# Performance work log

Measured on AMD Instinct MI355X. Metric: run time of the kernel, lower is better.

## Reference

```python
import jax, jax.numpy as jnp
import numpy as np

N_EMBD = 1024
N_HEAD = 16
B, T = 4, 2048

def setup_inputs() -> dict:
    key = jax.random.key(0)
    ks = jax.random.split(key, 5)
    C = N_EMBD
    s = 0.02
    return {
        "x": jax.random.normal(ks[0], (B, T, C), dtype=jnp.float32),
        "W_attn": jax.random.normal(ks[1], (C, 3 * C), dtype=jnp.float32) * s,
        "b_attn": jnp.zeros((3 * C,), dtype=jnp.float32),
        "W_proj": jax.random.normal(ks[2], (C, C), dtype=jnp.float32) * s,
        "b_proj": jnp.zeros((C,), dtype=jnp.float32),
    }

def reference(x, W_attn, b_attn, W_proj, b_proj):
    Bz, Tz, C = x.shape
    H = N_HEAD
    hd = C // H
    qkv = x @ W_attn + b_attn                      # [B,T,3C]
    q, k, v = jnp.split(qkv, 3, axis=-1)
    # [B,H,T,hd]
    q = q.reshape(Bz, Tz, H, hd).transpose(0, 2, 1, 3)
    k = k.reshape(Bz, Tz, H, hd).transpose(0, 2, 1, 3)
    v = v.reshape(Bz, Tz, H, hd).transpose(0, 2, 1, 3)
    att = jnp.einsum('bhqd,bhkd->bhqk', q, k) * (1.0 / np.sqrt(hd))
    causal = jnp.tril(jnp.ones((Tz, Tz), dtype=bool))
    att = jnp.where(causal, att, -jnp.inf)
    att = jax.nn.softmax(att, axis=-1)
    y = jnp.einsum('bhqk,bhkd->bhqd', att, v)      # [B,H,T,hd]
    y = y.transpose(0, 2, 1, 3).reshape(Bz, Tz, C)
    return y @ W_proj + b_proj
```

## Files before the change

### kernel.cpp

```cpp
#include <hip/hip_runtime.h>
#include <hip/hip_bf16.h>

#define NEMBD 1024
#define NHEAD 16
#define HD    64
#define BB    4
#define TT    2048
#define MM    (BB*TT)
#define NQKV  (3*NEMBD)

typedef unsigned short u16;
typedef __attribute__((ext_vector_type(8))) short short8;
typedef __attribute__((ext_vector_type(4))) float floatx4;

__device__ __forceinline__ u16 f2bf(float f) {
    __hip_bfloat16 h = __float2bfloat16(f);
    return *reinterpret_cast<u16*>(&h);
}

__device__ __forceinline__ unsigned pack_bf16(float a, float b) {
    __hip_bfloat162 h2 = __float22bfloat162_rn(float2{a, b});
    return *reinterpret_cast<unsigned*>(&h2);
}

__device__ __forceinline__ void gl_lds16(const u16* g, u16* l) {
    __builtin_amdgcn_global_load_lds(
        (const __attribute__((address_space(1))) unsigned int*)g,
        (__attribute__((address_space(3))) unsigned int*)l,
        16, 0, 0);
}

__global__ __launch_bounds__(256) void cast_f32_bf16(const float* __restrict__ in,
                                                     u16* __restrict__ out, int n) {
    int i = (blockIdx.x * 256 + threadIdx.x) * 4;
    if (i < n) {
        float4 v = *(const float4*)(in + i);
        uint2 o;
        o.x = pack_bf16(v.x, v.y);
        o.y = pack_bf16(v.z, v.w);
        *(uint2*)(out + i) = o;
    }
}

__global__ __launch_bounds__(256) void transpose_cast(const float* __restrict__ in,
                                                      u16* __restrict__ out, int K, int N) {
    __shared__ float tile[32][33];
    int n0 = blockIdx.x * 32, k0 = blockIdx.y * 32;
    int tx = threadIdx.x, ty = threadIdx.y;
    for (int i = 0; i < 4; i++)
        tile[ty + i * 8][tx] = in[(k0 + ty + i * 8) * N + n0 + tx];
    __syncthreads();
    for (int i = 0; i < 4; i++)
        out[(n0 + ty + i * 8) * K + k0 + tx] = f2bf(tile[tx][ty + i * 8]);
}

template <int EPI>
__global__ __launch_bounds__(256)
void gemm_bt(const u16* __restrict__ A, const u16* __restrict__ Bt,
             const float* __restrict__ bias, void* __restrict__ out0,
             u16* __restrict__ outK, u16* __restrict__ outV) {
    const int K = NEMBD;
    __shared__ u16 As[128 * 32];
    __shared__ u16 Bs[128 * 32];
    int tid = threadIdx.x;
    int lane = tid & 63, w = tid >> 6;
    int quad = lane >> 4, l16 = lane & 15;
    int wm = w >> 1, wn = w & 1;
    int bM = blockIdx.y * 128, bN = blockIdx.x * 128;

    floatx4 acc[4][4];
    for (int i = 0; i < 4; i++)
        for (int j = 0; j < 4; j++)
            acc[i][j] = (floatx4){0.f, 0.f, 0.f, 0.f};

    int srow = lane >> 2, scol = (lane & 3) * 8;
    const u16* Ag0 = A  + (size_t)(bM + w * 32 + srow) * K + scol;
    const u16* Ag1 = A  + (size_t)(bM + w * 32 + 16 + srow) * K + scol;
    const u16* Bg0 = Bt + (size_t)(bN + w * 32 + srow) * K + scol;
    const u16* Bg1 = Bt + (size_t)(bN + w * 32 + 16 + srow) * K + scol;
    u16* LA0 = &As[(w * 32) * 32];
    u16* LA1 = &As[(w * 32 + 16) * 32];
    u16* LB0 = &Bs[(w * 32) * 32];
    u16* LB1 = &Bs[(w * 32 + 16) * 32];

    for (int k0 = 0; k0 < K; k0 += 32) {
        gl_lds16(Ag0 + k0, LA0);
        gl_lds16(Ag1 + k0, LA1);
        gl_lds16(Bg0 + k0, LB0);
        gl_lds16(Bg1 + k0, LB1);
        __syncthreads();
        short8 af[4], bf[4];
        for (int i = 0; i < 4; i++)
            af[i] = *(const short8*)&As[(wm * 64 + i * 16 + l16) * 32 + quad * 8];
        for (int j = 0; j < 4; j++)
            bf[j] = *(const short8*)&Bs[(wn * 64 + j * 16 + l16) * 32 + quad * 8];
        for (int i = 0; i < 4; i++)
            for (int j = 0; j < 4; j++)
                acc[i][j] = __builtin_amdgcn_mfma_f32_16x16x32_bf16(af[i], bf[j], acc[i][j], 0, 0, 0);
        __syncthreads();
    }

    for (int i = 0; i < 4; i++) {
        int mbase = bM + wm * 64 + i * 16 + quad * 4;
        for (int j = 0; j < 4; j++) {
            int n = bN + wn * 64 + j * 16 + l16;
            float bv = bias[n];
            for (int r = 0; r < 4; r++) {
                float v = acc[i][j][r] + bv;
                int mg = mbase + r;
                if (EPI == 0) {
                    int which = n >> 10, c = n & 1023;
                    int h = c >> 6, d = c & 63;
                    int b = mg >> 11, t = mg & 2047;
                    u16* dst = (which == 0) ? (u16*)out0 : (which == 1 ? outK : outV);
                    dst[(((size_t)(b * NHEAD + h) * TT) + t) * HD + d] = f2bf(v);
                } else {
                    ((float*)out0)[(size_t)mg * NEMBD + n] = v;
                }
            }
        }
    }
}

__global__ __launch_bounds__(256)
void attn_kernel(const u16* __restrict__ Q, const u16* __restrict__ Kg,
                 const u16* __restrict__ V, u16* __restrict__ Y) {
    __shared__ u16 Ks[64][72];
    __shared__ u16 Vt[64][72];
    __shared__ u16 Ps[4][32][40];

    int tid = threadIdx.x;
    int lane = tid & 63, w = tid >> 6;
    int quad = lane >> 4, l16 = lane & 15;
    int bh = blockIdx.y;
    int ib = blockIdx.x;
    int qa0 = ib * 128;
    int qb0 = (15 - ib) * 128;
    const u16* Qb = Q  + (size_t)bh * TT * HD;
    const u16* Kb = Kg + (size_t)bh * TT * HD;
    const u16* Vb = V  + (size_t)bh * TT * HD;
    int wqa = qa0 + w * 32;
    int wqb = qb0 + w * 32;

    short8 qfa[2][2], qfb[2][2];
    for (int qt = 0; qt < 2; qt++)
        for (int kd = 0; kd < 2; kd++) {
            qfa[qt][kd] = *(const short8*)(Qb + (size_t)(wqa + qt * 16 + l16) * HD + kd * 32 + quad * 8);
            qfb[qt][kd] = *(const short8*)(Qb + (size_t)(wqb + qt * 16 + l16) * HD + kd * 32 + quad * 8);
        }

    floatx4 oa[4][2], ob[4][2];
    for (int dt = 0; dt < 4; dt++)
        for (int qt = 0; qt < 2; qt++) {
            oa[dt][qt] = (floatx4){0.f, 0.f, 0.f, 0.f};
            ob[dt][qt] = (floatx4){0.f, 0.f, 0.f, 0.f};
        }
    float la[2] = {0.f, 0.f};
    float lb[2] = {0.f, 0.f};

    const float C = 0.18033688f;

    int krow = tid >> 2, kcg = (tid & 3) * 16;
    int vkp = (tid & 31) * 2, vd0 = (tid >> 5) * 8;

    auto process = [&](int k0, int wq0, short8 (&qf)[2][2], floatx4 (&o)[4][2],
                       float (&l_s)[2]) {
        if (k0 >= wq0 + 32) return;
        short8 kf[4][2];
        for (int kt = 0; kt < 4; kt++)
            for (int kd = 0; kd < 2; kd++)
                kf[kt][kd] = *(const short8*)&Ks[kt * 16 + l16][kd * 32 + quad * 8];
        floatx4 s[2][4];
        for (int qt = 0; qt < 2; qt++)
            for (int kt = 0; kt < 4; kt++) {
                floatx4 a = (floatx4){0.f, 0.f, 0.f, 0.f};
                a = __builtin_amdgcn_mfma_f32_16x16x32_bf16(kf[kt][0], qf[qt][0], a, 0, 0, 0);
                a = __builtin_amdgcn_mfma_f32_16x16x32_bf16(kf[kt][1], qf[qt][1], a, 0, 0, 0);
                s[qt][kt] = a;
            }

        bool diag = (k0 + 64 > wq0);
        for (int qt = 0; qt < 2; qt++) {
            int qg = wq0 + qt * 16 + l16;
            if (diag) {
                for (int kt = 0; kt < 4; kt++)
                    for (int r = 0; r < 4; r++)
                        if (k0 + kt * 16 + quad * 4 + r > qg) s[qt][kt][r] = -INFINITY;
            }
            float rs = 0.f;
            for (int kt = 0; kt < 4; kt++)
                for (int r = 0; r < 4; r++) {
                    float p = exp2f(s[qt][kt][r] * C);
                    s[qt][kt][r] = p;
                    rs += p;
                }
            l_s[qt] += rs;
        }

        for (int c = 0; c < 2; c++) {
            for (int qt = 0; qt < 2; qt++)
                for (int ktl = 0; ktl < 2; ktl++) {
                    floatx4 p = s[qt][c * 2 + ktl];
                    *(unsigned*)&Ps[w][qt * 16 + l16][ktl * 16 + quad * 4]     = pack_bf16(p[0], p[1]);
                    *(unsigned*)&Ps[w][qt * 16 + l16][ktl * 16 + quad * 4 + 2] = pack_bf16(p[2], p[3]);
                }
            short8 pfrag[2];
            for (int qt = 0; qt < 2; qt++)
                pfrag[qt] = *(const short8*)&Ps[w][qt * 16 + l16][quad * 8];
            for (int dt = 0; dt < 4; dt++) {
                short8 vfrag = *(const short8*)&Vt[dt * 16 + l16][c * 32 + quad * 8];
                for (int qt = 0; qt < 2; qt++)
                    o[dt][qt] = __builtin_amdgcn_mfma_f32_16x16x32_bf16(vfrag, pfrag[qt], o[dt][qt], 0, 0, 0);
            }
        }
    };

    int kend = qb0 + 128;
    for (int k0 = 0; k0 < kend; k0 += 64) {
        *(uint4*)&Ks[krow][kcg]     = *(const uint4*)(Kb + (size_t)(k0 + krow) * HD + kcg);
        *(uint4*)&Ks[krow][kcg + 8] = *(const uint4*)(Kb + (size_t)(k0 + krow) * HD + kcg + 8);
        uint4 v0 = *(const uint4*)(Vb + (size_t)(k0 + vkp) * HD + vd0);
        uint4 v1 = *(const uint4*)(Vb + (size_t)(k0 + vkp + 1) * HD + vd0);
        const u16* e0 = (const u16*)&v0;
        const u16* e1 = (const u16*)&v1;
        for (int e = 0; e < 8; e++) {
            unsigned pk = (unsigned)e0[e] | ((unsigned)e1[e] << 16);
            *(unsigned*)&Vt[vd0 + e][vkp] = pk;
        }
        __syncthreads();

        if (k0 < qa0 + 128) process(k0, wqa, qfa, oa, la);
        process(k0, wqb, qfb, ob, lb);

        __syncthreads();
    }

    int b = bh >> 4, h = bh & 15;
    for (int half = 0; half < 2; half++) {
        floatx4 (&o)[4][2] = half ? ob : oa;
        float* l_s = half ? lb : la;
        int wq0 = half ? wqb : wqa;
        for (int qt = 0; qt < 2; qt++) {
            float lt = l_s[qt];
            lt += __shfl_xor(lt, 16, 64);
            lt += __shfl_xor(lt, 32, 64);
            float inv = 1.0f / lt;
            int qg = wq0 + qt * 16 + l16;
            size_t base = ((size_t)(b * TT + qg)) * NEMBD + h * HD;
            for (int dt = 0; dt < 4; dt++) {
                *(unsigned*)&Y[base + dt * 16 + quad * 4]     = pack_bf16(o[dt][qt][0] * inv, o[dt][qt][1] * inv);
                *(unsigned*)&Y[base + dt * 16 + quad * 4 + 2] = pack_bf16(o[dt][qt][2] * inv, o[dt][qt][3] * inv);
            }
        }
    }
}

extern "C" void kernel_launch(void* const* d_in, const int* in_sizes, int n_in,
                              void* d_out, int out_size, void* d_ws, size_t ws_size,
                              hipStream_t stream) {
    const float* x      = (const float*)d_in[0];
    const float* W_attn = (const float*)d_in[1];
    const float* b_attn = (const float*)d_in[2];
    const float* W_proj = (const float*)d_in[3];
    const float* b_proj = (const float*)d_in[4];
    float* out = (float*)d_out;

    char* ws = (char*)d_ws;
    u16* xb  = (u16*)(ws + 0);
    u16* wat = (u16*)(ws + 16777216);
    u16* wpt = (u16*)(ws + 23068672);
    u16* Qb  = (u16*)(ws + 25165824);
    u16* Kb  = (u16*)(ws + 41943040);
    u16* Vb  = (u16*)(ws + 58720256);

    cast_f32_bf16<<<(MM * NEMBD / 4 + 255) / 256, 256, 0, stream>>>(x, xb, MM * NEMBD);
    dim3 tb(32, 8);
    transpose_cast<<<dim3(NQKV / 32, NEMBD / 32), tb, 0, stream>>>(W_attn, wat, NEMBD, NQKV);
    transpose_cast<<<dim3(NEMBD / 32, NEMBD / 32), tb, 0, stream>>>(W_proj, wpt, NEMBD, NEMBD);

    gemm_bt<0><<<dim3(NQKV / 128, MM / 128), 256, 0, stream>>>(xb, wat, b_attn, (void*)Qb, Kb, Vb);
    attn_kernel<<<dim3(8, BB * NHEAD), 256, 0, stream>>>(Qb, Kb, Vb, xb);
    gemm_bt<1><<<dim3(NEMBD / 128, MM / 128), 256, 0, stream>>>(xb, wpt, b_proj, (void*)out, nullptr, nullptr);
}
```

Before: 284.8 us.

## Prescale Q, share K fragments, truncate P packing, and use perm for V transpose

Folds the softmax scale into Q fragments once at load time so the inner loop's exp2 skips the per-element multiply. K fragments are read from LDS once per tile and shared by both query halves, and the P tile is written to LDS in a single pass using truncation packing via byte-permute instead of round-to-nearest. The V transpose uses byte-permute instead of per-element shifts, and the launch bound requests two blocks per CU. Rounding Q after scaling and truncating P slightly change numerics, and the larger Ps buffer raises LDS use.

```diff
diff --git a/kernel.cpp b/kernel.cpp
--- a/kernel.cpp
+++ b/kernel.cpp
@@ -23,11 +23,26 @@
     return *reinterpret_cast<unsigned*>(&h2);
 }
 
+__device__ __forceinline__ unsigned trunc_pack(float a, float b) {
+    return __builtin_amdgcn_perm(__float_as_uint(b), __float_as_uint(a), 0x07060302u);
+}
+
 __device__ __forceinline__ void gl_lds16(const u16* g, u16* l) {
     __builtin_amdgcn_global_load_lds(
         (const __attribute__((address_space(1))) unsigned int*)g,
         (__attribute__((address_space(3))) unsigned int*)l,
         16, 0, 0);
+}
+
+__device__ __forceinline__ short8 scale8(short8 f, float c) {
+    union { short8 s; unsigned u[4]; } a, r;
+    a.s = f;
+    for (int i = 0; i < 4; i++) {
+        float lo = __uint_as_float(a.u[i] << 16) * c;
+        float hi = __uint_as_float(a.u[i] & 0xffff0000u) * c;
+        r.u[i] = pack_bf16(lo, hi);
+    }
+    return r.s;
 }
 
 __global__ __launch_bounds__(256) void cast_f32_bf16(const float* __restrict__ in,
@@ -122,12 +137,12 @@
     }
 }
 
-__global__ __launch_bounds__(256)
+__global__ __launch_bounds__(256, 2)
 void attn_kernel(const u16* __restrict__ Q, const u16* __restrict__ Kg,
                  const u16* __restrict__ V, u16* __restrict__ Y) {
     __shared__ u16 Ks[64][72];
     __shared__ u16 Vt[64][72];
-    __shared__ u16 Ps[4][32][40];
+    __shared__ u16 Ps[4][32][72];
 
     int tid = threadIdx.x;
     int lane = tid & 63, w = tid >> 6;
@@ -142,11 +157,13 @@
     int wqa = qa0 + w * 32;
     int wqb = qb0 + w * 32;
 
+    const float C = 0.18033688f;
+
     short8 qfa[2][2], qfb[2][2];
     for (int qt = 0; qt < 2; qt++)
         for (int kd = 0; kd < 2; kd++) {
-            qfa[qt][kd] = *(const short8*)(Qb + (size_t)(wqa + qt * 16 + l16) * HD + kd * 32 + quad * 8);
-            qfb[qt][kd] = *(const short8*)(Qb + (size_t)(wqb + qt * 16 + l16) * HD + kd * 32 + quad * 8);
+            qfa[qt][kd] = scale8(*(const short8*)(Qb + (size_t)(wqa + qt * 16 + l16) * HD + kd * 32 + quad * 8), C);
+            qfb[qt][kd] = scale8(*(const short8*)(Qb + (size_t)(wqb + qt * 16 + l16) * HD + kd * 32 + quad * 8), C);
         }
 
     floatx4 oa[4][2], ob[4][2];
@@ -158,18 +175,11 @@
     float la[2] = {0.f, 0.f};
     float lb[2] = {0.f, 0.f};
 
-    const float C = 0.18033688f;
-
     int krow = tid >> 2, kcg = (tid & 3) * 16;
     int vkp = (tid & 31) * 2, vd0 = (tid >> 5) * 8;
 
-    auto process = [&](int k0, int wq0, short8 (&qf)[2][2], floatx4 (&o)[4][2],
-                       float (&l_s)[2]) {
-        if (k0 >= wq0 + 32) return;
-        short8 kf[4][2];
-        for (int kt = 0; kt < 4; kt++)
-            for (int kd = 0; kd < 2; kd++)
-                kf[kt][kd] = *(const short8*)&Ks[kt * 16 + l16][kd * 32 + quad * 8];
+    auto process = [&](int k0, int wq0, short8 (&qf)[2][2], short8 (&kf)[4][2],
+                       floatx4 (&o)[4][2], float (&l_s)[2]) {
         floatx4 s[2][4];
         for (int qt = 0; qt < 2; qt++)
             for (int kt = 0; kt < 4; kt++) {
@@ -190,29 +200,29 @@
             float rs = 0.f;
             for (int kt = 0; kt < 4; kt++)
                 for (int r = 0; r < 4; r++) {
-                    float p = exp2f(s[qt][kt][r] * C);
+                    float p = exp2f(s[qt][kt][r]);
                     s[qt][kt][r] = p;
                     rs += p;
                 }
             l_s[qt] += rs;
         }
 
-        for (int c = 0; c < 2; c++) {
-            for (int qt = 0; qt < 2; qt++)
-                for (int ktl = 0; ktl < 2; ktl++) {
-                    floatx4 p = s[qt][c * 2 + ktl];
-                    *(unsigned*)&Ps[w][qt * 16 + l16][ktl * 16 + quad * 4]     = pack_bf16(p[0], p[1]);
-                    *(unsigned*)&Ps[w][qt * 16 + l16][ktl * 16 + quad * 4 + 2] = pack_bf16(p[2], p[3]);
-                }
-            short8 pfrag[2];
-            for (int qt = 0; qt < 2; qt++)
-                pfrag[qt] = *(const short8*)&Ps[w][qt * 16 + l16][quad * 8];
+        for (int qt = 0; qt < 2; qt++)
+            for (int kt = 0; kt < 4; kt++) {
+                floatx4 p = s[qt][kt];
+                *(unsigned*)&Ps[w][qt * 16 + l16][kt * 16 + quad * 4]     = trunc_pack(p[0], p[1]);
+                *(unsigned*)&Ps[w][qt * 16 + l16][kt * 16 + quad * 4 + 2] = trunc_pack(p[2], p[3]);
+            }
+        short8 pfrag[2][2];
+        for (int qt = 0; qt < 2; qt++)
+            for (int c = 0; c < 2; c++)
+                pfrag[qt][c] = *(const short8*)&Ps[w][qt * 16 + l16][c * 32 + quad * 8];
+        for (int c = 0; c < 2; c++)
             for (int dt = 0; dt < 4; dt++) {
                 short8 vfrag = *(const short8*)&Vt[dt * 16 + l16][c * 32 + quad * 8];
                 for (int qt = 0; qt < 2; qt++)
-                    o[dt][qt] = __builtin_amdgcn_mfma_f32_16x16x32_bf16(vfrag, pfrag[qt], o[dt][qt], 0, 0, 0);
-            }
-        }
+                    o[dt][qt] = __builtin_amdgcn_mfma_f32_16x16x32_bf16(vfrag, pfrag[qt][c], o[dt][qt], 0, 0, 0);
+            }
     };
 
     int kend = qb0 + 128;
@@ -221,17 +231,24 @@
         *(uint4*)&Ks[krow][kcg + 8] = *(const uint4*)(Kb + (size_t)(k0 + krow) * HD + kcg + 8);
         uint4 v0 = *(const uint4*)(Vb + (size_t)(k0 + vkp) * HD + vd0);
         uint4 v1 = *(const uint4*)(Vb + (size_t)(k0 + vkp + 1) * HD + vd0);
-        const u16* e0 = (const u16*)&v0;
-        const u16* e1 = (const u16*)&v1;
-        for (int e = 0; e < 8; e++) {
-            unsigned pk = (unsigned)e0[e] | ((unsigned)e1[e] << 16);
-            *(unsigned*)&Vt[vd0 + e][vkp] = pk;
+        const unsigned* w0p = (const unsigned*)&v0;
+        const unsigned* w1p = (const unsigned*)&v1;
+        for (int e = 0; e < 4; e++) {
+            *(unsigned*)&Vt[vd0 + 2 * e][vkp]     = __builtin_amdgcn_perm(w1p[e], w0p[e], 0x05040100u);
+            *(unsigned*)&Vt[vd0 + 2 * e + 1][vkp] = __builtin_amdgcn_perm(w1p[e], w0p[e], 0x07060302u);
         }
         __syncthreads();
 
-        if (k0 < qa0 + 128) process(k0, wqa, qfa, oa, la);
-        process(k0, wqb, qfb, ob, lb);
-
+        bool acta = (k0 < qa0 + 128) && (k0 < wqa + 32);
+        bool actb = (k0 < wqb + 32);
+        if (acta || actb) {
+            short8 kf[4][2];
+            for (int kt = 0; kt < 4; kt++)
+                for (int kd = 0; kd < 2; kd++)
+                    kf[kt][kd] = *(const short8*)&Ks[kt * 16 + l16][kd * 32 + quad * 8];
+            if (acta) process(k0, wqa, qfa, kf, oa, la);
+            if (actb) process(k0, wqb, qfb, kf, ob, lb);
+        }
         __syncthreads();
     }
 
```

New measurement: 269.4 us. 5.4% less time.
